# Kernel optimization log

Measured on AMD Instinct MI355X. Metric: run time of the kernel, lower is better.

The kernel has to match this reference:

```python
import jax, jax.numpy as jnp
import numpy as np

IN_F = 4096
OUT_F = 11008
RANK = 16
LORA_SCALE = 2.0
VALS_PER_WORD = 16


def pack_int2(T):
    """Pack ternary T in {-1,0,+1} [out, in] into int32 [out, in//16] (code = T+1)."""
    out_f, in_f = T.shape
    codes = (T + 1).astype(jnp.int32).reshape(out_f, in_f // VALS_PER_WORD, VALS_PER_WORD)
    shifts = (jnp.arange(VALS_PER_WORD, dtype=jnp.int32) * 2)
    # disjoint bit fields -> sum == bitwise OR
    return jnp.sum(codes << shifts, axis=-1).astype(jnp.int32)


def unpack_int2(packed, in_features, dtype):
    """Unpack int32 [out, nblk] -> ternary [out, in_features] in given dtype."""
    shifts = (jnp.arange(VALS_PER_WORD, dtype=jnp.int32) * 2)
    codes = (packed[:, :, None] >> shifts) & 3  # [out, nblk, 16]
    T = codes.reshape(packed.shape[0], -1)[:, :in_features]
    return T.astype(dtype) - jnp.asarray(1, dtype)


def setup_inputs() -> dict:
    key = jax.random.key(0)
    k_x, k_t, k_a, k_m, k_b, k_la, k_lb = jax.random.split(key, 7)
    x = jax.random.normal(k_x, (256, IN_F), dtype=jnp.float32)
    # random ternary weights, packed faithfully (code = T + 1)
    T = jax.random.randint(k_t, (OUT_F, IN_F), -1, 2, dtype=jnp.int32)
    int2_packed = pack_int2(T)
    alpha = jax.random.uniform(k_a, (OUT_F,), dtype=jnp.float32, minval=0.01, maxval=0.05)
    mu = jax.random.normal(k_m, (OUT_F,), dtype=jnp.float32) * 0.001
    bias = jax.random.normal(k_b, (OUT_F,), dtype=jnp.float32) * 0.02
    lora_A = jax.random.normal(k_la, (RANK, IN_F), dtype=jnp.float32) * (1.0 / np.sqrt(IN_F))
    lora_B = jax.random.normal(k_lb, (OUT_F, RANK), dtype=jnp.float32) * 0.01
    return {"x": x, "int2_packed": int2_packed, "alpha": alpha, "mu": mu,
            "bias": bias, "lora_A": lora_A, "lora_B": lora_B}


def reference(x, int2_packed, alpha, mu, bias, lora_A, lora_B):
    # unpack INT2 -> ternary weight matrix in activation dtype
    T = unpack_int2(int2_packed, IN_F, x.dtype)          # [out, in]
    ternary_out = jnp.einsum('mi,oi->mo', x, T)          # F.linear(x, T)
    ternary_out = ternary_out * alpha                    # per-row scale
    # asymmetric shift: mu_o * sum_i x_i
    ternary_out = ternary_out + mu * jnp.sum(x, axis=-1, keepdims=True)
    # LoRA correction: scale * (x A^T) B^T
    lora_out = jnp.einsum('mr,or->mo', jnp.einsum('mi,ri->mr', x, lora_A), lora_B)
    ternary_out = ternary_out + LORA_SCALE * lora_out
    return ternary_out + bias
```

## Files before the change

### kernel.cpp

```cpp
#include <hip/hip_runtime.h>
#include <stdint.h>

#define IN_F 4096
#define OUT_F 11008
#define M_ROWS 256
#define RANK 16
#define NWORDS (IN_F / 16)

#define BM 64
#define BN 64
#define BK 64
#define NIT (IN_F / BK)

typedef unsigned short u16;
typedef __attribute__((ext_vector_type(8))) short short8;
typedef __attribute__((ext_vector_type(4))) float floatx4;

__device__ __forceinline__ u16 f32_to_bf16_rne(float f) {
    uint32_t u = __builtin_bit_cast(uint32_t, f);
    uint32_t r = (u + 0x7FFFu + ((u >> 16) & 1u)) >> 16;
    return (u16)r;
}

__global__ __launch_bounds__(256) void prep_kernel(
    const float* __restrict__ x, const float* __restrict__ lora_A,
    u16* __restrict__ xb, float* __restrict__ srow, float* __restrict__ lxa)
{
    const int m = blockIdx.x;
    const int tid = threadIdx.x;
    const float4* xrow4 = (const float4*)(x + (size_t)m * IN_F);
    const float4* la4 = (const float4*)lora_A;
    float ssum = 0.f;
    float acc[RANK];
#pragma unroll
    for (int r = 0; r < RANK; ++r) acc[r] = 0.f;
#pragma unroll
    for (int t = 0; t < IN_F / (256 * 4); ++t) {
        int i4 = t * 256 + tid;
        float4 v = xrow4[i4];
        ssum += v.x + v.y + v.z + v.w;
        union { u16 h[4]; uint2 u2; } pk;
        pk.h[0] = f32_to_bf16_rne(v.x);
        pk.h[1] = f32_to_bf16_rne(v.y);
        pk.h[2] = f32_to_bf16_rne(v.z);
        pk.h[3] = f32_to_bf16_rne(v.w);
        *(uint2*)&xb[(size_t)m * IN_F + i4 * 4] = pk.u2;
#pragma unroll
        for (int r = 0; r < RANK; ++r) {
            float4 a = la4[r * (IN_F / 4) + i4];
            acc[r] = fmaf(v.x, a.x, fmaf(v.y, a.y, fmaf(v.z, a.z, fmaf(v.w, a.w, acc[r]))));
        }
    }
#pragma unroll
    for (int off = 32; off > 0; off >>= 1) {
        ssum += __shfl_down(ssum, off, 64);
#pragma unroll
        for (int r = 0; r < RANK; ++r) acc[r] += __shfl_down(acc[r], off, 64);
    }
    __shared__ float red[4][RANK + 1];
    int wv = tid >> 6, ln = tid & 63;
    if (ln == 0) {
        red[wv][0] = ssum;
#pragma unroll
        for (int r = 0; r < RANK; ++r) red[wv][1 + r] = acc[r];
    }
    __syncthreads();
    if (tid == 0) srow[m] = red[0][0] + red[1][0] + red[2][0] + red[3][0];
    if (tid < RANK)
        lxa[m * RANK + tid] = red[0][1 + tid] + red[1][1 + tid] + red[2][1 + tid] + red[3][1 + tid];
}

__device__ __forceinline__ short8 decode8(uint32_t h)
{
    uint32_t selA = (h & 0xFu) | ((h & 0xF0u) << 12);
    selA = (selA | (selA << 6)) & 0x03030303u;
    uint32_t h2 = h >> 8;
    uint32_t selB = (h2 & 0xFu) | ((h2 & 0xF0u) << 12);
    selB = (selB | (selB << 6)) & 0x03030303u;
    uint32_t hiA = __builtin_amdgcn_perm(0u, 0x003F00BFu, selA);
    uint32_t loA = __builtin_amdgcn_perm(0u, 0x00800080u, selA);
    uint32_t hiB = __builtin_amdgcn_perm(0u, 0x003F00BFu, selB);
    uint32_t loB = __builtin_amdgcn_perm(0u, 0x00800080u, selB);
    union { uint32_t u[4]; short8 s; } cvt;
    cvt.u[0] = __builtin_amdgcn_perm(hiA, loA, 0x05010400u);
    cvt.u[1] = __builtin_amdgcn_perm(hiA, loA, 0x07030602u);
    cvt.u[2] = __builtin_amdgcn_perm(hiB, loB, 0x05010400u);
    cvt.u[3] = __builtin_amdgcn_perm(hiB, loB, 0x07030602u);
    return cvt.s;
}

#define WAITV6 asm volatile("s_waitcnt vmcnt(6)" ::: "memory")
#define WAITV3 asm volatile("s_waitcnt vmcnt(3)" ::: "memory")
#define WAITV0 asm volatile("s_waitcnt vmcnt(0)" ::: "memory")

__global__ __launch_bounds__(256, 4) void gemm_kernel(
    const u16* __restrict__ xb, const uint32_t* __restrict__ Tp,
    const float* __restrict__ alpha, const float* __restrict__ mu,
    const float* __restrict__ bias, const float* __restrict__ lora_B,
    const float* __restrict__ srow, const float* __restrict__ lxa,
    float* __restrict__ out)
{
    __shared__ __align__(16) u16 ldsA[4][BM * BK];
    __shared__ __align__(16) uint32_t ldsB[4][BN * 4];

    const int tid = threadIdx.x;
    const int lane = tid & 63;
    const int wave = tid >> 6;
    const int wm = wave >> 1, wn = wave & 1;
    const int mb = blockIdx.y * BM;
    const int nb = blockIdx.x * BN;

    const int bshift = ((lane >> 4) & 1) * 16;

    const u16* asrc[2];
    int adst[2];
#pragma unroll
    for (int j = 0; j < 2; ++j) {
        int q = j * 256 + tid;
        int row = q >> 3;
        int scc = (q & 7) ^ (row & 7);
        asrc[j] = xb + (size_t)(mb + row) * IN_F + scc * 8;
        adst[j] = q * 8;
    }
    const uint32_t* bsrc = Tp + (size_t)(nb + lane) * NWORDS;
    const int bdst = lane * 4;

    floatx4 acc[2][2] = {};

    auto stage = [&](int buf, int git) {
        const int k0 = git * BK;
#pragma unroll
        for (int j = 0; j < 2; ++j) {
            __builtin_amdgcn_global_load_lds(
                (const __attribute__((address_space(1))) void*)(asrc[j] + k0),
                (__attribute__((address_space(3))) void*)(&ldsA[buf][adst[j]]),
                16, 0, 0);
        }
        __builtin_amdgcn_global_load_lds(
            (const __attribute__((address_space(1))) void*)(bsrc + git * 4),
            (__attribute__((address_space(3))) void*)(&ldsB[buf][bdst]),
            16, 0, 0);
    };

    auto body = [&](int buf, int buf_next, int git_next, bool do_stage) {
        if (do_stage) stage(buf_next, git_next);
        __builtin_amdgcn_sched_barrier(0);
        short8 af[2][2];
        uint32_t bwd[2][2];
#pragma unroll
        for (int mt = 0; mt < 2; ++mt) {
            int r = wm * 32 + mt * 16 + (lane & 15);
#pragma unroll
            for (int kk = 0; kk < 2; ++kk) {
                int sc = kk * 4 + (lane >> 4);
                int chunk = r * 8 + (sc ^ (r & 7));
                af[mt][kk] = *(const short8*)&ldsA[buf][chunk * 8];
            }
        }
#pragma unroll
        for (int nt = 0; nt < 2; ++nt) {
            int row = wn * 32 + nt * 16 + (lane & 15);
#pragma unroll
            for (int kk = 0; kk < 2; ++kk)
                bwd[nt][kk] = ldsB[buf][row * 4 + kk * 2 + (lane >> 5)];
        }
        __builtin_amdgcn_s_setprio(1);
#pragma unroll
        for (int kk = 0; kk < 2; ++kk) {
            short8 bf[2];
#pragma unroll
            for (int nt = 0; nt < 2; ++nt)
                bf[nt] = decode8((bwd[nt][kk] >> bshift) & 0xFFFFu);
#pragma unroll
            for (int mt = 0; mt < 2; ++mt)
#pragma unroll
                for (int nt = 0; nt < 2; ++nt)
                    acc[mt][nt] = __builtin_amdgcn_mfma_f32_16x16x32_bf16(
                        af[mt][kk], bf[nt], acc[mt][nt], 0, 0, 0);
        }
        __builtin_amdgcn_s_setprio(0);
    };

    stage(0, 0);
    stage(1, 1);
    stage(2, 2);

    for (int j = 0; j <= NIT - 4; ++j) {
        WAITV6;
        __builtin_amdgcn_s_barrier();
        body(j & 3, (j + 3) & 3, j + 3, true);
    }
    WAITV6; __builtin_amdgcn_s_barrier();
    body((NIT - 3) & 3, 0, 0, false);
    WAITV3; __builtin_amdgcn_s_barrier();
    body((NIT - 2) & 3, 0, 0, false);
    WAITV0; __builtin_amdgcn_s_barrier();
    body((NIT - 1) & 3, 0, 0, false);

    const int o0 = nb + wn * 32 + (lane & 15);
    const int m0 = mb + wm * 32 + ((lane >> 4) * 4);

    float al[2], muv[2], bi[2], Brow[2][RANK];
#pragma unroll
    for (int nt = 0; nt < 2; ++nt) {
        int o = o0 + nt * 16;
        al[nt] = alpha[o];
        muv[nt] = mu[o];
        bi[nt] = bias[o];
        const float4* b4 = (const float4*)(lora_B + (size_t)o * RANK);
#pragma unroll
        for (int r4 = 0; r4 < RANK / 4; ++r4) {
            float4 v = b4[r4];
            Brow[nt][r4 * 4 + 0] = v.x; Brow[nt][r4 * 4 + 1] = v.y;
            Brow[nt][r4 * 4 + 2] = v.z; Brow[nt][r4 * 4 + 3] = v.w;
        }
    }
#pragma unroll
    for (int mt = 0; mt < 2; ++mt) {
#pragma unroll
        for (int rg = 0; rg < 4; ++rg) {
            int m = m0 + mt * 16 + rg;
            float sm = srow[m];
            float lx[RANK];
            const float4* l4 = (const float4*)(lxa + (size_t)m * RANK);
#pragma unroll
            for (int r4 = 0; r4 < RANK / 4; ++r4) {
                float4 v = l4[r4];
                lx[r4 * 4 + 0] = v.x; lx[r4 * 4 + 1] = v.y;
                lx[r4 * 4 + 2] = v.z; lx[r4 * 4 + 3] = v.w;
            }
#pragma unroll
            for (int nt = 0; nt < 2; ++nt) {
                float lora = 0.f;
#pragma unroll
                for (int r = 0; r < RANK; ++r) lora = fmaf(lx[r], Brow[nt][r], lora);
                out[(size_t)m * OUT_F + o0 + nt * 16] =
                    al[nt] * acc[mt][nt][rg] + muv[nt] * sm + 2.0f * lora + bi[nt];
            }
        }
    }
}

extern "C" void kernel_launch(void* const* d_in, const int* in_sizes, int n_in,
                              void* d_out, int out_size, void* d_ws, size_t ws_size,
                              hipStream_t stream)
{
    const float* x = (const float*)d_in[0];
    const uint32_t* Tp = (const uint32_t*)d_in[1];
    const float* alpha = (const float*)d_in[2];
    const float* mu = (const float*)d_in[3];
    const float* bias = (const float*)d_in[4];
    const float* lora_A = (const float*)d_in[5];
    const float* lora_B = (const float*)d_in[6];
    float* out = (float*)d_out;

    u16* xb = (u16*)d_ws;
    float* srow = (float*)((char*)d_ws + (size_t)M_ROWS * IN_F * 2);
    float* lxa = (float*)((char*)d_ws + (size_t)M_ROWS * IN_F * 2 + 4096);

    prep_kernel<<<dim3(M_ROWS), dim3(256), 0, stream>>>(x, lora_A, xb, srow, lxa);
    gemm_kernel<<<dim3(OUT_F / BN, M_ROWS / BM), dim3(256), 0, stream>>>(
        xb, Tp, alpha, mu, bias, lora_B, srow, lxa, out);
}
```

Baseline: 77.38 us.

## Double-buffer register fragments so LDS reads overlap the MFMA compute

Splits the loop body into fragment reads and compute, and keeps two register fragment sets. The LDS reads for the next K-tile are issued right after the barrier, while the MFMAs for the current tile are still in flight. The loop is unrolled by four to rotate the LDS buffers, and the swizzled LDS offsets are precomputed once outside the loop. The aim is to hide LDS read latency behind MFMA work, at the cost of more VGPRs under the occupancy bound of 4.

Measured after the change: 62.61 us. 1.24x faster.

```diff
diff --git a/kernel.cpp b/kernel.cpp
--- a/kernel.cpp
+++ b/kernel.cpp
@@ -92,6 +92,13 @@
 #define WAITV6 asm volatile("s_waitcnt vmcnt(6)" ::: "memory")
 #define WAITV3 asm volatile("s_waitcnt vmcnt(3)" ::: "memory")
 #define WAITV0 asm volatile("s_waitcnt vmcnt(0)" ::: "memory")
+#define BAR    __builtin_amdgcn_s_barrier()
+#define SCHED0 __builtin_amdgcn_sched_barrier(0)
+
+struct Frags {
+    short8 af[2][2];
+    uint32_t bwd[2][2];
+};
 
 __global__ __launch_bounds__(256, 4) void gemm_kernel(
     const u16* __restrict__ xb, const uint32_t* __restrict__ Tp,
@@ -125,6 +132,23 @@
     const uint32_t* bsrc = Tp + (size_t)(nb + lane) * NWORDS;
     const int bdst = lane * 4;
 
+    int aoff[2][2], boff[2][2];
+#pragma unroll
+    for (int mt = 0; mt < 2; ++mt)
+#pragma unroll
+        for (int kk = 0; kk < 2; ++kk) {
+            int r = wm * 32 + mt * 16 + (lane & 15);
+            int sc = kk * 4 + (lane >> 4);
+            aoff[mt][kk] = (r * 8 + (sc ^ (r & 7))) * 8;
+        }
+#pragma unroll
+    for (int nt = 0; nt < 2; ++nt)
+#pragma unroll
+        for (int kk = 0; kk < 2; ++kk) {
+            int row = wn * 32 + nt * 16 + (lane & 15);
+            boff[nt][kk] = row * 4 + kk * 2 + (lane >> 5);
+        }
+
     floatx4 acc[2][2] = {};
 
     auto stage = [&](int buf, int git) {
@@ -142,60 +166,56 @@
             16, 0, 0);
     };
 
-    auto body = [&](int buf, int buf_next, int git_next, bool do_stage) {
-        if (do_stage) stage(buf_next, git_next);
-        __builtin_amdgcn_sched_barrier(0);
-        short8 af[2][2];
-        uint32_t bwd[2][2];
-#pragma unroll
-        for (int mt = 0; mt < 2; ++mt) {
-            int r = wm * 32 + mt * 16 + (lane & 15);
-#pragma unroll
-            for (int kk = 0; kk < 2; ++kk) {
-                int sc = kk * 4 + (lane >> 4);
-                int chunk = r * 8 + (sc ^ (r & 7));
-                af[mt][kk] = *(const short8*)&ldsA[buf][chunk * 8];
-            }
-        }
-#pragma unroll
-        for (int nt = 0; nt < 2; ++nt) {
-            int row = wn * 32 + nt * 16 + (lane & 15);
+    auto rdfrags = [&](int buf, Frags& F) {
+#pragma unroll
+        for (int mt = 0; mt < 2; ++mt)
 #pragma unroll
             for (int kk = 0; kk < 2; ++kk)
-                bwd[nt][kk] = ldsB[buf][row * 4 + kk * 2 + (lane >> 5)];
-        }
+                F.af[mt][kk] = *(const short8*)&ldsA[buf][aoff[mt][kk]];
+#pragma unroll
+        for (int nt = 0; nt < 2; ++nt)
+#pragma unroll
+            for (int kk = 0; kk < 2; ++kk)
+                F.bwd[nt][kk] = ldsB[buf][boff[nt][kk]];
+    };
+
+    auto compute = [&](Frags& F) {
         __builtin_amdgcn_s_setprio(1);
 #pragma unroll
         for (int kk = 0; kk < 2; ++kk) {
             short8 bf[2];
 #pragma unroll
             for (int nt = 0; nt < 2; ++nt)
-                bf[nt] = decode8((bwd[nt][kk] >> bshift) & 0xFFFFu);
+                bf[nt] = decode8((F.bwd[nt][kk] >> bshift) & 0xFFFFu);
 #pragma unroll
             for (int mt = 0; mt < 2; ++mt)
 #pragma unroll
                 for (int nt = 0; nt < 2; ++nt)
                     acc[mt][nt] = __builtin_amdgcn_mfma_f32_16x16x32_bf16(
-                        af[mt][kk], bf[nt], acc[mt][nt], 0, 0, 0);
+                        F.af[mt][kk], bf[nt], acc[mt][nt], 0, 0, 0);
         }
         __builtin_amdgcn_s_setprio(0);
     };
+
+    Frags fA, fB;
 
     stage(0, 0);
     stage(1, 1);
     stage(2, 2);
-
-    for (int j = 0; j <= NIT - 4; ++j) {
-        WAITV6;
-        __builtin_amdgcn_s_barrier();
-        body(j & 3, (j + 3) & 3, j + 3, true);
-    }
-    WAITV6; __builtin_amdgcn_s_barrier();
-    body((NIT - 3) & 3, 0, 0, false);
-    WAITV3; __builtin_amdgcn_s_barrier();
-    body((NIT - 2) & 3, 0, 0, false);
-    WAITV0; __builtin_amdgcn_s_barrier();
-    body((NIT - 1) & 3, 0, 0, false);
+    WAITV6; BAR;
+    rdfrags(0, fA); SCHED0;
+
+    for (int u = 0; u < 15; ++u) {
+        const int jb = u * 4;
+        stage(3, jb + 3); SCHED0; compute(fA); WAITV6; BAR; rdfrags(1, fB); SCHED0;
+        stage(0, jb + 4); SCHED0; compute(fB); WAITV6; BAR; rdfrags(2, fA); SCHED0;
+        stage(1, jb + 5); SCHED0; compute(fA); WAITV6; BAR; rdfrags(3, fB); SCHED0;
+        stage(2, jb + 6); SCHED0; compute(fB); WAITV6; BAR; rdfrags(0, fA); SCHED0;
+    }
+    stage(3, 63); SCHED0; compute(fA); WAITV6; BAR; rdfrags(1, fB); SCHED0;
+    compute(fB); WAITV3; BAR; rdfrags(2, fA); SCHED0;
+    compute(fA); WAITV0; BAR; rdfrags(3, fB); SCHED0;
+    compute(fB);
 
     const int o0 = nb + wn * 32 + (lane & 15);
     const int m0 = mb + wm * 32 + ((lane >> 4) * 4);
```
